# Optimization experiments

Hardware: AMD Instinct MI355X
Metric: run time of the kernel (lower is better)

Reference implementation:

```python
import jax, jax.numpy as jnp
import numpy as np

B, N, K = 8, 4096, 64          # graphs, nodes per graph, clusters
E_PER = 65536                   # edges per graph (avg degree 16)
EPS = 1e-15


def gcn_conv(x, W, b, src, dst, num_nodes):
    """PyG GCNConv: add self-loops, symmetric deg^-1/2 normalization, sum-aggregate at dst."""
    h = x @ W
    loop = jnp.arange(num_nodes, dtype=src.dtype)
    s_all = jnp.concatenate([src, loop])
    d_all = jnp.concatenate([dst, loop])
    deg = jax.ops.segment_sum(jnp.ones(d_all.shape[0], dtype=h.dtype), d_all, num_segments=num_nodes)
    dis = jnp.where(deg > 0, jax.lax.rsqrt(deg), 0.0)
    msg = h[s_all] * (dis[s_all] * dis[d_all])[:, None]
    return jax.ops.segment_sum(msg, d_all, num_segments=num_nodes) + b


def setup_inputs() -> dict:
    key = jax.random.key(0)
    ks = jax.random.split(key, 12)
    F_in, H, F_out = 128, 128, 128
    x = jax.random.normal(ks[0], (B * N, F_in), dtype=jnp.float32)
    # within-graph random edges, then offset to global node ids
    local = jax.random.randint(ks[1], (2, B * E_PER), 0, N, dtype=jnp.int32)
    offs = jnp.repeat(jnp.arange(B, dtype=jnp.int32) * N, E_PER)
    edge_index = local + offs[None, :]
    batch = jnp.repeat(jnp.arange(B, dtype=jnp.int32), N)

    def lin(k, i, o):
        return (jax.random.normal(k, (i, o), dtype=jnp.float32) / np.float32(np.sqrt(i)))

    return {
        "x": x, "edge_index": edge_index, "batch": batch,
        "W1": lin(ks[2], F_in, H), "b1": jnp.zeros((H,), jnp.float32),
        "W2": lin(ks[3], H, H),    "b2": jnp.zeros((H,), jnp.float32),
        "Wa1": lin(ks[4], H, H),   "ba1": jnp.zeros((H,), jnp.float32),
        "Wa2": lin(ks[5], H, K),   "ba2": jnp.zeros((K,), jnp.float32),
        "Wo": lin(ks[6], H, F_out), "bo": jnp.zeros((F_out,), jnp.float32),
    }


def reference(x, edge_index, batch, W1, b1, W2, b2, Wa1, ba1, Wa2, ba2, Wo, bo):
    num_nodes = B * N
    src, dst = edge_index[0], edge_index[1]
    # two GCN layers (dropout inactive in eval mode)
    h = jax.nn.relu(gcn_conv(x, W1, b1, src, dst, num_nodes))
    h = gcn_conv(h, W2, b2, src, dst, num_nodes)
    # assignment MLP + softmax (module applies softmax; dense_mincut_pool re-applies it)
    s = jax.nn.softmax(jnp.tanh(h @ Wa1 + ba1) @ Wa2 + ba2, axis=-1)
    # to_dense_adj: scatter edges into [B, N, N]
    g = src // N
    adj = jnp.zeros((B, N, N), h.dtype).at[g, src % N, dst % N].add(1.0)
    # to_dense_batch: equal-size graphs -> reshape (mask all True)
    x_d = h.reshape(B, N, -1)
    s_d = jax.nn.softmax(s.reshape(B, N, K), axis=-1)  # PyG internal softmax (double softmax, faithful)
    # dense_mincut_pool
    out = jnp.einsum('bnk,bnf->bkf', s_d, x_d)              # s^T x : [B,K,F]
    As = jnp.einsum('bnm,bmk->bnk', adj, s_d)
    out_adj = jnp.einsum('bnk,bnj->bkj', s_d, As)           # s^T A s : [B,K,K]
    mincut_num = jnp.trace(out_adj, axis1=-2, axis2=-1)
    d_flat = adj.sum(-1)                                    # node degrees
    mincut_den = jnp.einsum('bnk,bn,bnk->b', s_d, d_flat, s_d)  # trace(s^T D s)
    mincut_loss = jnp.mean(-(mincut_num / mincut_den))
    ss = jnp.einsum('bnk,bnj->bkj', s_d, s_d)
    ss_n = jnp.linalg.norm(ss, axis=(-1, -2), keepdims=True)
    i_s = jnp.eye(K, dtype=ss.dtype)
    ortho_loss = jnp.mean(jnp.linalg.norm(ss / ss_n - i_s / jnp.sqrt(jnp.float32(K)), axis=(-1, -2)))
    # zero diagonal + symmetric degree normalization of pooled adj
    out_adj = out_adj * (1.0 - i_s)
    d = jnp.sqrt(out_adj.sum(-1))[:, None, :] + EPS         # [B,1,K]
    out_adj = out_adj / d / jnp.swapaxes(d, 1, 2)
    # output projection
    pooled_x = jax.nn.relu(out.reshape(-1, out.shape[-1]) @ Wo + bo)  # [B*K, F_out]
    pooled_batch = jnp.repeat(jnp.arange(B), K)
    # pooled_adj returned densely: pooled_edge_index == nonzero(pooled_adj > 0) (dynamic shape)
    return pooled_x, out_adj, pooled_batch, mincut_loss, ortho_loss
```

## Files before the change

### kernel.cpp

```cpp
#include <hip/hip_runtime.h>

#define NNODES 32768
#define NEDGES 524288
#define KCL 64
#define CPG 16

typedef _Float16 half8v __attribute__((ext_vector_type(8)));
typedef _Float16 half4v __attribute__((ext_vector_type(4)));
typedef float floatx4 __attribute__((ext_vector_type(4)));

#define WT1_OFF   0
#define WT2_OFF   16384
#define WTA1_OFF  32768
#define WTA2_OFF  49152
#define WTO_OFF   57344
#define WT_TOTAL  73728

__device__ __forceinline__ float wave_sum(float v) {
#pragma unroll
  for (int off = 32; off > 0; off >>= 1) v += __shfl_xor(v, off, 64);
  return v;
}

__global__ __launch_bounds__(256) void histgemm1_kernel(const int* __restrict__ src, const int* __restrict__ dst,
                                                        int* __restrict__ pIn,
                                                        const float* __restrict__ W1, const float* __restrict__ W2,
                                                        const float* __restrict__ Wa1, const float* __restrict__ Wa2,
                                                        const float* __restrict__ Wo, _Float16* __restrict__ wt16,
                                                        const float* __restrict__ x, _Float16* __restrict__ h16A,
                                                        float* __restrict__ out) {
  __shared__ _Float16 WT[128][136];
  const int t = threadIdx.x;
  if (blockIdx.x < 128) {
    int* hIn = reinterpret_cast<int*>(&WT[0][0]);
    const int g = blockIdx.x & 7;
    const int chunk = blockIdx.x >> 3;
    const int ebase = (g << 16) + (chunk << 12);
    const int nbase = g << 12;
    if (blockIdx.x == 0 && t < 2) out[98816 + t] = 0.f;
    for (int i = t; i < 4096; i += 256) hIn[i] = 0;
    __syncthreads();
    {
      int tg = blockIdx.x * 256 + t;
#pragma unroll
      for (int i = 0; i < 3; i++) {
        int id = tg + i * 32768;
        if (id < WT_TOTAL) {
          const float* W; int base, BN;
          if (id < 16384)      { W = W1;  base = WT1_OFF;  BN = 128; }
          else if (id < 32768) { W = W2;  base = WT2_OFF;  BN = 128; }
          else if (id < 49152) { W = Wa1; base = WTA1_OFF; BN = 128; }
          else if (id < 57344) { W = Wa2; base = WTA2_OFF; BN = 64; }
          else                 { W = Wo;  base = WTO_OFF;  BN = 128; }
          int m = id - base;
          int k = m / BN, n = m % BN;
          wt16[base + n * 128 + k] = (_Float16)W[m];
        }
      }
    }
    const int4* dst4 = reinterpret_cast<const int4*>(dst + ebase);
#pragma unroll
    for (int i = 0; i < 4; ++i) {
      int4 d = dst4[i * 256 + t];
      atomicAdd(&hIn[d.x - nbase], 1);
      atomicAdd(&hIn[d.y - nbase], 1);
      atomicAdd(&hIn[d.z - nbase], 1);
      atomicAdd(&hIn[d.w - nbase], 1);
    }
    __syncthreads();
    int* dIn = pIn + ((size_t)(g * CPG + chunk) << 12);
    for (int i = t; i < 4096; i += 256) dIn[i] = hIn[i];
  } else {
    const int bid = blockIdx.x - 128;
    const int lane = t & 63;
    const int quad = lane >> 4, l16 = lane & 15;
    const long rowbase = (long)(bid & 7) * 4096 + (long)(bid >> 3) * 128 + (t >> 6) * 32;
    half8v af[2][4];
#pragma unroll
    for (int rt = 0; rt < 2; rt++)
#pragma unroll
      for (int kt = 0; kt < 4; kt++) {
        const float* p = x + (rowbase + rt * 16 + l16) * 128 + kt * 32 + quad * 8;
        float4 p0 = *reinterpret_cast<const float4*>(p);
        float4 p1 = *reinterpret_cast<const float4*>(p + 4);
        half8v h = {(_Float16)p0.x, (_Float16)p0.y, (_Float16)p0.z, (_Float16)p0.w,
                    (_Float16)p1.x, (_Float16)p1.y, (_Float16)p1.z, (_Float16)p1.w};
        af[rt][kt] = h;
      }
#pragma unroll
    for (int i = 0; i < 16; i++) {
      int idx = i * 256 + t;
      int k = idx >> 5, n4 = (idx & 31) << 2;
      float4 wv = *reinterpret_cast<const float4*>(W1 + k * 128 + n4);
      WT[n4 + 0][k] = (_Float16)wv.x;
      WT[n4 + 1][k] = (_Float16)wv.y;
      WT[n4 + 2][k] = (_Float16)wv.z;
      WT[n4 + 3][k] = (_Float16)wv.w;
    }
    __syncthreads();
    floatx4 acc[2][8];
#pragma unroll
    for (int rt = 0; rt < 2; rt++)
#pragma unroll
      for (int ct = 0; ct < 8; ct++) acc[rt][ct] = {0.f, 0.f, 0.f, 0.f};
#pragma unroll
    for (int kt = 0; kt < 4; kt++) {
      half8v bf[8];
#pragma unroll
      for (int ct = 0; ct < 8; ct++)
        bf[ct] = *reinterpret_cast<const half8v*>(&WT[ct * 16 + l16][kt * 32 + quad * 8]);
#pragma unroll
      for (int rt = 0; rt < 2; rt++)
#pragma unroll
        for (int ct = 0; ct < 8; ct++)
          acc[rt][ct] = __builtin_amdgcn_mfma_f32_16x16x32_f16(af[rt][kt], bf[ct], acc[rt][ct], 0, 0, 0);
    }
#pragma unroll
    for (int rt = 0; rt < 2; rt++) {
#pragma unroll
      for (int r = 0; r < 4; r++) {
        long row = rowbase + rt * 16 + quad * 4 + r;
#pragma unroll
        for (int ct = 0; ct < 8; ct++)
          h16A[row * 128 + ct * 16 + l16] = (_Float16)acc[rt][ct][r];
      }
    }
  }
}

__global__ __launch_bounds__(1024) void scan2_kernel(const int* __restrict__ pIn, int* __restrict__ offs,
                                                     int* __restrict__ cbase, float* __restrict__ dis) {
  __shared__ int part[1024];
  const int t = threadIdx.x;
  const int g = blockIdx.x;
  int tot[4];
  int s = 0;
#pragma unroll
  for (int j = 0; j < 4; ++j) {
    int l = t * 4 + j;
    int cnt = 0;
#pragma unroll
    for (int c = 0; c < CPG; ++c) cnt += pIn[(((size_t)(g * CPG + c)) << 12) + l];
    tot[j] = cnt;
    s += cnt;
  }
  part[t] = s;
  __syncthreads();
  for (int off = 1; off < 1024; off <<= 1) {
    int add = (t >= off) ? part[t - off] : 0;
    __syncthreads();
    part[t] += add;
    __syncthreads();
  }
  int run = (g << 16) + ((t == 0) ? 0 : part[t - 1]);
#pragma unroll
  for (int j = 0; j < 4; ++j) {
    int l = t * 4 + j;
    int n = (g << 12) + l;
    offs[n] = run;
    dis[n] = rsqrtf((float)tot[j] + 1.0f);
    int running = run;
#pragma unroll
    for (int c = 0; c < CPG; ++c) {
      size_t idx = (((size_t)(g * CPG + c)) << 12) + l;
      cbase[idx] = running;
      running += pIn[idx];
    }
    run += tot[j];
  }
  if (g == 0 && t == 0) offs[NNODES] = NEDGES;
}

__global__ __launch_bounds__(256) void scatter2_kernel(const int* __restrict__ src, const int* __restrict__ dst,
                                                       const int* __restrict__ cbase, int* __restrict__ ssrc) {
  __shared__ int cur[4096];
  const int t = threadIdx.x;
  const int g = blockIdx.x & 7;
  const int chunk = blockIdx.x >> 3;
  const int ebase = (g << 16) + (chunk << 12);
  const int nbase = g << 12;
  const int* cb = cbase + ((size_t)(g * CPG + chunk) << 12);
  for (int i = t; i < 4096; i += 256) cur[i] = cb[i];
  __syncthreads();
  const int4* dst4 = reinterpret_cast<const int4*>(dst + ebase);
  const int4* src4 = reinterpret_cast<const int4*>(src + ebase);
#pragma unroll
  for (int i = 0; i < 4; ++i) {
    int4 d = dst4[i * 256 + t];
    int4 s = src4[i * 256 + t];
    int p0 = atomicAdd(&cur[d.x - nbase], 1); ssrc[p0] = s.x;
    int p1 = atomicAdd(&cur[d.y - nbase], 1); ssrc[p1] = s.y;
    int p2 = atomicAdd(&cur[d.z - nbase], 1); ssrc[p2] = s.z;
    int p3 = atomicAdd(&cur[d.w - nbase], 1); ssrc[p3] = s.w;
  }
}

template <int ACT, int BIAS, int SCALE, int AFP32>
__global__ __launch_bounds__(256) void mgemm_kernel(const void* __restrict__ Ain, const _Float16* __restrict__ WT16,
                                                    const float* __restrict__ bias, const float* __restrict__ rowscale,
                                                    _Float16* __restrict__ Cout) {
  __shared__ _Float16 WT[128][136];
  const int t = threadIdx.x;
  const int lane = t & 63;
  const int quad = lane >> 4, l16 = lane & 15;
  const long rowbase = (long)(blockIdx.x & 7) * 4096 + (long)(blockIdx.x >> 3) * 128 + (t >> 6) * 32;
  half8v af[2][4];
#pragma unroll
  for (int rt = 0; rt < 2; rt++)
#pragma unroll
    for (int kt = 0; kt < 4; kt++) {
      if (AFP32) {
        const float* A32 = (const float*)Ain;
        const float* p = A32 + (rowbase + rt * 16 + l16) * 128 + kt * 32 + quad * 8;
        float4 p0 = *reinterpret_cast<const float4*>(p);
        float4 p1 = *reinterpret_cast<const float4*>(p + 4);
        half8v h = {(_Float16)p0.x, (_Float16)p0.y, (_Float16)p0.z, (_Float16)p0.w,
                    (_Float16)p1.x, (_Float16)p1.y, (_Float16)p1.z, (_Float16)p1.w};
        af[rt][kt] = h;
      } else {
        const _Float16* A16 = (const _Float16*)Ain;
        af[rt][kt] = *reinterpret_cast<const half8v*>(A16 + (rowbase + rt * 16 + l16) * 128 + kt * 32 + quad * 8);
      }
    }
#pragma unroll
  for (int i = 0; i < 8; i++) {
    int idx = i * 256 + t;
    int n = idx >> 4, k8 = (idx & 15) << 3;
    *reinterpret_cast<half8v*>(&WT[n][k8]) = *reinterpret_cast<const half8v*>(&WT16[n * 128 + k8]);
  }
  __syncthreads();
  floatx4 acc[2][8];
#pragma unroll
  for (int rt = 0; rt < 2; rt++)
#pragma unroll
    for (int ct = 0; ct < 8; ct++) acc[rt][ct] = {0.f, 0.f, 0.f, 0.f};
#pragma unroll
  for (int kt = 0; kt < 4; kt++) {
    half8v bf[8];
#pragma unroll
    for (int ct = 0; ct < 8; ct++)
      bf[ct] = *reinterpret_cast<const half8v*>(&WT[ct * 16 + l16][kt * 32 + quad * 8]);
#pragma unroll
    for (int rt = 0; rt < 2; rt++)
#pragma unroll
      for (int ct = 0; ct < 8; ct++)
        acc[rt][ct] = __builtin_amdgcn_mfma_f32_16x16x32_f16(af[rt][kt], bf[ct], acc[rt][ct], 0, 0, 0);
  }
#pragma unroll
  for (int rt = 0; rt < 2; rt++) {
#pragma unroll
    for (int r = 0; r < 4; r++) {
      long row = rowbase + rt * 16 + quad * 4 + r;
      float sc = SCALE ? rowscale[row] : 1.f;
#pragma unroll
      for (int ct = 0; ct < 8; ct++) {
        float v = acc[rt][ct][r];
        if (SCALE) v *= sc;
        if (BIAS) v += bias[ct * 16 + l16];
        if (ACT == 1) v = fmaxf(v, 0.f);
        Cout[row * 128 + ct * 16 + l16] = (_Float16)v;
      }
    }
  }
}

__global__ __launch_bounds__(256) void mlp_kernel(const _Float16* __restrict__ h2, const _Float16* __restrict__ wta1,
                                                  const _Float16* __restrict__ wta2, const float* __restrict__ ba1,
                                                  const float* __restrict__ ba2, _Float16* __restrict__ sh) {
  __shared__ _Float16 WT1[128][136];
  __shared__ _Float16 Z[64][136];
  const int t = threadIdx.x;
  const int lane = t & 63;
  const int quad = lane >> 4, l16 = lane & 15;
  const int w = t >> 6;
  const long rowbase = (long)(blockIdx.x & 7) * 4096 + (long)(blockIdx.x >> 3) * 64 + w * 16;
  half8v af[4];
#pragma unroll
  for (int kt = 0; kt < 4; kt++)
    af[kt] = *reinterpret_cast<const half8v*>(h2 + (rowbase + l16) * 128 + kt * 32 + quad * 8);
#pragma unroll
  for (int i = 0; i < 8; i++) {
    int idx = i * 256 + t;
    int n = idx >> 4, k8 = (idx & 15) << 3;
    *reinterpret_cast<half8v*>(&WT1[n][k8]) = *reinterpret_cast<const half8v*>(&wta1[n * 128 + k8]);
  }
  __syncthreads();
  {
    floatx4 acc[8];
#pragma unroll
    for (int ct = 0; ct < 8; ct++) acc[ct] = {0.f, 0.f, 0.f, 0.f};
#pragma unroll
    for (int kt = 0; kt < 4; kt++) {
#pragma unroll
      for (int ct = 0; ct < 8; ct++) {
        half8v bf = *reinterpret_cast<const half8v*>(&WT1[ct * 16 + l16][kt * 32 + quad * 8]);
        acc[ct] = __builtin_amdgcn_mfma_f32_16x16x32_f16(af[kt], bf, acc[ct], 0, 0, 0);
      }
    }
#pragma unroll
    for (int r = 0; r < 4; r++) {
      int lrow = w * 16 + quad * 4 + r;
#pragma unroll
      for (int ct = 0; ct < 8; ct++) {
        float zx = acc[ct][r] + ba1[ct * 16 + l16];
        float ex = __expf(2.0f * zx);
        float v = 1.0f - 2.0f * __builtin_amdgcn_rcpf(ex + 1.0f);
        Z[lrow][ct * 16 + l16] = (_Float16)v;
      }
    }
  }
  __syncthreads();
#pragma unroll
  for (int i = 0; i < 4; i++) {
    int idx = i * 256 + t;
    int n = idx >> 4, k8 = (idx & 15) << 3;
    *reinterpret_cast<half8v*>(&WT1[n][k8]) = *reinterpret_cast<const half8v*>(&wta2[n * 128 + k8]);
  }
  half8v af2[4];
#pragma unroll
  for (int kt = 0; kt < 4; kt++)
    af2[kt] = *reinterpret_cast<const half8v*>(&Z[w * 16 + l16][kt * 32 + quad * 8]);
  __syncthreads();
  floatx4 acc2[4];
#pragma unroll
  for (int ct = 0; ct < 4; ct++) acc2[ct] = {0.f, 0.f, 0.f, 0.f};
#pragma unroll
  for (int kt = 0; kt < 4; kt++) {
#pragma unroll
    for (int ct = 0; ct < 4; ct++) {
      half8v bf = *reinterpret_cast<const half8v*>(&WT1[ct * 16 + l16][kt * 32 + quad * 8]);
      acc2[ct] = __builtin_amdgcn_mfma_f32_16x16x32_f16(af2[kt], bf, acc2[ct], 0, 0, 0);
    }
  }
#pragma unroll
  for (int r = 0; r < 4; r++) {
    long row = rowbase + quad * 4 + r;
    float v[4];
#pragma unroll
    for (int ct = 0; ct < 4; ct++) v[ct] = acc2[ct][r] + ba2[ct * 16 + l16];
    float m = fmaxf(fmaxf(v[0], v[1]), fmaxf(v[2], v[3]));
#pragma unroll
    for (int off = 1; off <= 8; off <<= 1) m = fmaxf(m, __shfl_xor(m, off, 64));
    float se = 0.f;
#pragma unroll
    for (int ct = 0; ct < 4; ct++) { v[ct] = __expf(v[ct] - m); se += v[ct]; }
#pragma unroll
    for (int off = 1; off <= 8; off <<= 1) se += __shfl_xor(se, off, 64);
    float inv = 1.0f / se;
#pragma unroll
    for (int ct = 0; ct < 4; ct++) v[ct] *= inv;
    float m2 = fmaxf(fmaxf(v[0], v[1]), fmaxf(v[2], v[3]));
#pragma unroll
    for (int off = 1; off <= 8; off <<= 1) m2 = fmaxf(m2, __shfl_xor(m2, off, 64));
    float se2 = 0.f;
#pragma unroll
    for (int ct = 0; ct < 4; ct++) { v[ct] = __expf(v[ct] - m2); se2 += v[ct]; }
#pragma unroll
    for (int off = 1; off <= 8; off <<= 1) se2 += __shfl_xor(se2, off, 64);
    float inv2 = 1.0f / se2;
#pragma unroll
    for (int ct = 0; ct < 4; ct++) sh[row * 64 + ct * 16 + l16] = (_Float16)(v[ct] * inv2);
  }
}

template <int RELU, int DISSRC>
__global__ __launch_bounds__(256) void aggregate_kernel(const _Float16* __restrict__ hs, const float* __restrict__ dis,
                                                        const int* __restrict__ offs, const int* __restrict__ ssrc,
                                                        const float* __restrict__ bias, _Float16* __restrict__ outh) {
  const int lane = threadIdx.x & 63;
  const int b = blockIdx.x;
  const int node = ((b & 7) << 12) + ((b >> 3) << 2) + (threadIdx.x >> 6);
  const int q = lane >> 4;
  const int fl = (lane & 15) * 8;
  const int e0 = offs[node], e1 = offs[node + 1];
  const float dn = dis[node];
  float fa[8];
#pragma unroll
  for (int j = 0; j < 8; j++) fa[j] = 0.f;
  int e = e0;
  for (; e + 16 <= e1; e += 16) {
    int s0 = ssrc[e + q];
    int s1 = ssrc[e + 4 + q];
    int s2 = ssrc[e + 8 + q];
    int s3 = ssrc[e + 12 + q];
    float d0 = 1.f, d1 = 1.f, d2 = 1.f, d3 = 1.f;
    if (DISSRC) { d0 = dis[s0]; d1 = dis[s1]; d2 = dis[s2]; d3 = dis[s3]; }
    half8v v0 = *reinterpret_cast<const half8v*>(hs + (size_t)s0 * 128 + fl);
    half8v v1 = *reinterpret_cast<const half8v*>(hs + (size_t)s1 * 128 + fl);
    half8v v2 = *reinterpret_cast<const half8v*>(hs + (size_t)s2 * 128 + fl);
    half8v v3 = *reinterpret_cast<const half8v*>(hs + (size_t)s3 * 128 + fl);
#pragma unroll
    for (int j = 0; j < 8; j++) {
      if (DISSRC) {
        fa[j] = fmaf(d0, (float)v0[j], fa[j]);
        fa[j] = fmaf(d1, (float)v1[j], fa[j]);
        fa[j] = fmaf(d2, (float)v2[j], fa[j]);
        fa[j] = fmaf(d3, (float)v3[j], fa[j]);
      } else {
        fa[j] += (float)v0[j] + (float)v1[j] + (float)v2[j] + (float)v3[j];
      }
    }
  }
  if (e < e1) {
    int last = e1 - 1;
    int s[4]; bool m[4];
#pragma unroll
    for (int jj = 0; jj < 4; jj++) {
      int idx = e + jj * 4 + q;
      m[jj] = idx < e1;
      int sv = ssrc[idx < last ? idx : last];
      s[jj] = m[jj] ? sv : node;
    }
#pragma unroll
    for (int jj = 0; jj < 4; jj++) {
      half8v v = *reinterpret_cast<const half8v*>(hs + (size_t)s[jj] * 128 + fl);
      float ds = DISSRC ? dis[s[jj]] : 1.f;
      if (m[jj]) {
#pragma unroll
        for (int j = 0; j < 8; j++) {
          if (DISSRC) fa[j] = fmaf(ds, (float)v[j], fa[j]);
          else fa[j] += (float)v[j];
        }
      }
    }
  }
#pragma unroll
  for (int j = 0; j < 8; j++) {
    fa[j] += __shfl_xor(fa[j], 16, 64);
    fa[j] += __shfl_xor(fa[j], 32, 64);
  }
  if (q == 0) {
    half8v self = *reinterpret_cast<const half8v*>(hs + (size_t)node * 128 + fl);
    float4 b0 = *reinterpret_cast<const float4*>(bias + fl);
    float4 b1 = *reinterpret_cast<const float4*>(bias + fl + 4);
    float bb[8] = {b0.x, b0.y, b0.z, b0.w, b1.x, b1.y, b1.z, b1.w};
    half8v r;
#pragma unroll
    for (int j = 0; j < 8; j++) {
      float acc = fa[j];
      if (DISSRC) acc = fmaf(dn, (float)self[j], acc);
      else acc += (float)self[j];
      float v = fmaf(acc, dn, bb[j]);
      if (RELU) v = fmaxf(v, 0.f);
      r[j] = (_Float16)v;
    }
    *reinterpret_cast<half8v*>(outh + (size_t)node * 128 + fl) = r;
  }
}

__global__ __launch_bounds__(256) void gather_kernel(const _Float16* __restrict__ sh, const int* __restrict__ offs,
                                                     const int* __restrict__ ssrc, _Float16* __restrict__ Gh,
                                                     float* __restrict__ dnp) {
  const int lane = threadIdx.x & 63;
  const int b = blockIdx.x;
  const int node = ((b & 7) << 12) + ((b >> 3) << 2) + (threadIdx.x >> 6);
  const int q = lane >> 3;
  const int fl = (lane & 7) * 8;
  const int e0 = offs[node], e1 = offs[node + 1];
  float fa[8];
  float sq = 0.f;
#pragma unroll
  for (int j = 0; j < 8; j++) fa[j] = 0.f;
  int e = e0;
  for (; e + 16 <= e1; e += 16) {
    int s0 = ssrc[e + q];
    int s1 = ssrc[e + 8 + q];
    half8v v0 = *reinterpret_cast<const half8v*>(sh + (size_t)s0 * 64 + fl);
    half8v v1 = *reinterpret_cast<const half8v*>(sh + (size_t)s1 * 64 + fl);
#pragma unroll
    for (int j = 0; j < 8; j++) {
      float f0 = (float)v0[j], f1 = (float)v1[j];
      fa[j] += f0 + f1;
      sq = fmaf(f0, f0, sq);
      sq = fmaf(f1, f1, sq);
    }
  }
  if (e < e1) {
    int last = e1 - 1;
    int i0 = e + q, i1 = e + 8 + q;
    bool m0 = i0 < e1, m1 = i1 < e1;
    int sv0 = ssrc[i0 < last ? i0 : last];
    int sv1 = ssrc[i1 < last ? i1 : last];
    int s0 = m0 ? sv0 : node;
    int s1 = m1 ? sv1 : node;
    half8v v0 = *reinterpret_cast<const half8v*>(sh + (size_t)s0 * 64 + fl);
    half8v v1 = *reinterpret_cast<const half8v*>(sh + (size_t)s1 * 64 + fl);
#pragma unroll
    for (int j = 0; j < 8; j++) {
      float f0 = m0 ? (float)v0[j] : 0.f;
      float f1 = m1 ? (float)v1[j] : 0.f;
      fa[j] += f0 + f1;
      sq = fmaf(f0, f0, sq);
      sq = fmaf(f1, f1, sq);
    }
  }
#pragma unroll
  for (int j = 0; j < 8; j++) {
    fa[j] += __shfl_xor(fa[j], 8, 64);
    fa[j] += __shfl_xor(fa[j], 16, 64);
    fa[j] += __shfl_xor(fa[j], 32, 64);
  }
  float den = wave_sum(sq);
  if (lane == 0) dnp[node] = den;
  if (q == 0) {
    half8v r;
#pragma unroll
    for (int j = 0; j < 8; j++) r[j] = (_Float16)fa[j];
    *reinterpret_cast<half8v*>(Gh + (size_t)node * 64 + fl) = r;
  }
}

__global__ __launch_bounds__(512) void atb_kernel(const _Float16* __restrict__ sh, const _Float16* __restrict__ Gh,
                                                  const _Float16* __restrict__ h2, float* __restrict__ pF) {
  __shared__ _Float16 XsT[64][136];
  __shared__ _Float16 YsT[256][40];
  const int t = threadIdx.x;
  const int g = blockIdx.x & 7, chunk = blockIdx.x >> 3;
  const int n0 = g * 4096 + chunk * 128;
  const int lane = t & 63;
  const int w = t >> 6;
  const int mtile = w & 3;
  const int nhalf = w >> 2;
  const int quad = lane >> 4, l16 = lane & 15;

#pragma unroll
  for (int i = 0; i < 4; i++) {
    int slot = i * 512 + t;
    int k = slot >> 4, c4 = (slot & 15) * 4;
    half4v v = *reinterpret_cast<const half4v*>(&sh[(size_t)(n0 + k) * 64 + c4]);
#pragma unroll
    for (int j = 0; j < 4; j++) XsT[c4 + j][k] = v[j];
  }

  floatx4 acc[8];
#pragma unroll
  for (int nt = 0; nt < 8; nt++) acc[nt] = {0.f, 0.f, 0.f, 0.f};

  for (int kt = 0; kt < 4; ++kt) {
    const int nb = n0 + kt * 32;
    __syncthreads();
#pragma unroll
    for (int i = 0; i < 4; i++) {
      int slot = i * 512 + t;
      int cg = slot & 15, k = (slot >> 4) & 31, ch = slot >> 9;
      int c = ch * 64 + cg * 4;
      half4v v;
      if (c < 64)       v = *reinterpret_cast<const half4v*>(&Gh[(size_t)(nb + k) * 64 + c]);
      else if (c < 128) v = *reinterpret_cast<const half4v*>(&sh[(size_t)(nb + k) * 64 + (c - 64)]);
      else              v = *reinterpret_cast<const half4v*>(&h2[(size_t)(nb + k) * 128 + (c - 128)]);
#pragma unroll
      for (int j = 0; j < 4; j++) YsT[c + j][k] = v[j];
    }
    __syncthreads();
    half8v af = *reinterpret_cast<const half8v*>(&XsT[mtile * 16 + l16][kt * 32 + quad * 8]);
#pragma unroll
    for (int nt = 0; nt < 8; nt++) {
      half8v bf = *reinterpret_cast<const half8v*>(&YsT[(nhalf * 8 + nt) * 16 + l16][quad * 8]);
      acc[nt] = __builtin_amdgcn_mfma_f32_16x16x32_f16(af, bf, acc[nt], 0, 0, 0);
    }
  }
  float* dst = pF + (size_t)blockIdx.x * 16384;
#pragma unroll
  for (int nt = 0; nt < 8; nt++) {
#pragma unroll
    for (int r = 0; r < 4; r++) {
      dst[(mtile * 16 + quad * 4 + r) * 256 + (nhalf * 8 + nt) * 16 + l16] = acc[nt][r];
    }
  }
}

__global__ __launch_bounds__(256) void merge_kernel(const float* __restrict__ pF, float* __restrict__ oadj,
                                                    float* __restrict__ ssb, _Float16* __restrict__ outp16) {
  int g = blockIdx.x & 7;
  int o4 = (blockIdx.x >> 3) * 256 + threadIdx.x;
  float sx = 0.f, sy = 0.f, sz = 0.f, sw = 0.f;
#pragma unroll
  for (int q = 0; q < 32; ++q) {
    float4 v = *reinterpret_cast<const float4*>(pF + (size_t)(q * 8 + g) * 16384 + o4 * 4);
    sx += v.x; sy += v.y; sz += v.z; sw += v.w;
  }
  int row = o4 >> 6;
  int c = (o4 & 63) * 4;
  if (c < 64) {
    float4 o = {sx, sy, sz, sw};
    *reinterpret_cast<float4*>(&oadj[g * 4096 + row * 64 + c]) = o;
  } else if (c < 128) {
    float4 o = {sx, sy, sz, sw};
    *reinterpret_cast<float4*>(&ssb[g * 4096 + row * 64 + (c - 64)]) = o;
  } else {
    half4v h = {(_Float16)sx, (_Float16)sy, (_Float16)sz, (_Float16)sw};
    *reinterpret_cast<half4v*>(&outp16[g * 8192 + row * 128 + (c - 128)]) = h;
  }
}

__global__ __launch_bounds__(256) void epilogue2_kernel(const float* __restrict__ oadj, const float* __restrict__ ssb,
                                                        const _Float16* __restrict__ outp16, const _Float16* __restrict__ wto,
                                                        const float* __restrict__ bo, const float* __restrict__ dn,
                                                        float* __restrict__ out) {
  __shared__ _Float16 outpS[64][136];
  __shared__ _Float16 WoT[128][136];
  __shared__ float red[256];
  __shared__ float rowsum[64];
  __shared__ float dw[4], w1[4], w2[4], w3[4];
  const int g = blockIdx.x, t = threadIdx.x;

#pragma unroll
  for (int i = 0; i < 8; i++) {
    int idx = i * 256 + t;
    int n = idx >> 4, k8 = (idx & 15) << 3;
    *reinterpret_cast<half8v*>(&WoT[n][k8]) = *reinterpret_cast<const half8v*>(&wto[n * 128 + k8]);
  }
#pragma unroll
  for (int i = 0; i < 4; i++) {
    int idx = i * 256 + t;
    int orow = idx >> 4, c8 = (idx & 15) * 8;
    half8v v = *reinterpret_cast<const half8v*>(&outp16[g * 8192 + orow * 128 + c8]);
    *reinterpret_cast<half8v*>(&outpS[orow][c8]) = v;
  }

  const int row = t >> 2, p = t & 3;
  float Areg[16];
  float trs_p = 0.f, ssq_p = 0.f;
#pragma unroll
  for (int c4 = 0; c4 < 4; c4++) {
    float4 a = *reinterpret_cast<const float4*>(&oadj[g * 4096 + row * 64 + p * 16 + c4 * 4]);
    Areg[c4 * 4 + 0] = a.x; Areg[c4 * 4 + 1] = a.y; Areg[c4 * 4 + 2] = a.z; Areg[c4 * 4 + 3] = a.w;
    float4 s = *reinterpret_cast<const float4*>(&ssb[g * 4096 + row * 64 + p * 16 + c4 * 4]);
    float vv[4] = {s.x, s.y, s.z, s.w};
#pragma unroll
    for (int jj = 0; jj < 4; jj++) {
      ssq_p += vv[jj] * vv[jj];
      int col = p * 16 + c4 * 4 + jj;
      if (col == row) trs_p += vv[jj];
    }
  }
  float da = 0.f;
#pragma unroll
  for (int i = 0; i < 16; i++) da += dn[g * 4096 + i * 256 + t];
  float dws = wave_sum(da);
  if ((t & 63) == 0) dw[t >> 6] = dws;

  float rs = 0.f, tra = 0.f;
#pragma unroll
  for (int c = 0; c < 16; c++) {
    int j = p * 16 + c;
    if (j == row) tra += Areg[c];
    else rs += Areg[c];
  }
  red[t] = rs;
  __syncthreads();
  if (p == 0) rowsum[row] = red[t] + red[t + 1] + red[t + 2] + red[t + 3];
  float v1 = wave_sum(tra), v2 = wave_sum(trs_p), v3 = wave_sum(ssq_p);
  if ((t & 63) == 0) { int w = t >> 6; w1[w] = v1; w2[w] = v2; w3[w] = v3; }
  __syncthreads();
  if (t == 0) {
    float TRA = w1[0] + w1[1] + w1[2] + w1[3];
    float TRS = w2[0] + w2[1] + w2[2] + w2[3];
    float SSQ = w3[0] + w3[1] + w3[2] + w3[3];
    float DEN = dw[0] + dw[1] + dw[2] + dw[3];
    atomicAdd(&out[98816], -(TRA / DEN) * 0.125f);
    float ssn = sqrtf(SSQ);
    atomicAdd(&out[98817], sqrtf(2.0f - TRS / (4.0f * ssn)) * 0.125f);
  }
  float di = sqrtf(rowsum[row]) + 1e-15f;
#pragma unroll
  for (int c = 0; c < 16; c++) {
    int j = p * 16 + c;
    float v = (j == row) ? 0.f : Areg[c];
    float dj = sqrtf(rowsum[j]) + 1e-15f;
    out[65536 + g * 4096 + row * 64 + j] = v / (di * dj);
  }
  if (t < 64) out[98304 + g * 64 + t] = (float)g;

  const int lane = t & 63;
  const int quad = lane >> 4, l16 = lane & 15;
  const int w = t >> 6;
  floatx4 acc[8];
#pragma unroll
  for (int ct = 0; ct < 8; ct++) acc[ct] = {0.f, 0.f, 0.f, 0.f};
#pragma unroll
  for (int kt = 0; kt < 4; kt++) {
    half8v af = *reinterpret_cast<const half8v*>(&outpS[w * 16 + l16][kt * 32 + quad * 8]);
#pragma unroll
    for (int ct = 0; ct < 8; ct++) {
      half8v bf = *reinterpret_cast<const half8v*>(&WoT[ct * 16 + l16][kt * 32 + quad * 8]);
      acc[ct] = __builtin_amdgcn_mfma_f32_16x16x32_f16(af, bf, acc[ct], 0, 0, 0);
    }
  }
#pragma unroll
  for (int r = 0; r < 4; r++) {
    int orow = w * 16 + quad * 4 + r;
#pragma unroll
    for (int ct = 0; ct < 8; ct++) {
      int col = ct * 16 + l16;
      float v = fmaxf(acc[ct][r] + bo[col], 0.f);
      out[(g * 64 + orow) * 128 + col] = v;
    }
  }
}

extern "C" void kernel_launch(void* const* d_in, const int* in_sizes, int n_in,
                              void* d_out, int out_size, void* d_ws, size_t ws_size,
                              hipStream_t stream) {
  const float* x   = (const float*)d_in[0];
  const int*   ei  = (const int*)d_in[1];
  const float* W1  = (const float*)d_in[3];
  const float* b1  = (const float*)d_in[4];
  const float* W2  = (const float*)d_in[5];
  const float* b2  = (const float*)d_in[6];
  const float* Wa1 = (const float*)d_in[7];
  const float* ba1 = (const float*)d_in[8];
  const float* Wa2 = (const float*)d_in[9];
  const float* ba2 = (const float*)d_in[10];
  const float* Wo  = (const float*)d_in[11];
  const float* bo  = (const float*)d_in[12];
  const int* src = ei;
  const int* dst = ei + NEDGES;
  float* out = (float*)d_out;

  char* ws = (char*)d_ws;
  size_t o = 0;
  auto alloc = [&](size_t bytes) -> void* {
    void* p = ws + o;
    o += (bytes + 255) & ~(size_t)255;
    return p;
  };
  _Float16* h16A = (_Float16*)alloc((size_t)NNODES * 128 * 2);
  _Float16* h16B = (_Float16*)alloc((size_t)NNODES * 128 * 2);
  _Float16* h16C = (_Float16*)alloc((size_t)NNODES * 128 * 2);
  _Float16* sh   = (_Float16*)alloc((size_t)NNODES * 64 * 2);
  _Float16* Gh   = (_Float16*)alloc((size_t)NNODES * 64 * 2);
  float* pF    = (float*)alloc((size_t)256 * 16384 * 4);
  float* dis   = (float*)alloc((size_t)NNODES * 4);
  int* offs    = (int*)alloc((size_t)(NNODES + 1) * 4);
  int* ssrc    = (int*)alloc((size_t)NEDGES * 4);
  int* pIn     = (int*)alloc((size_t)8 * CPG * 4096 * 4);
  int* cbase   = (int*)alloc((size_t)8 * CPG * 4096 * 4);
  float* dn    = (float*)alloc((size_t)NNODES * 4);
  float* oadj  = (float*)alloc(8 * 4096 * 4);
  float* ssb   = (float*)alloc(8 * 4096 * 4);
  _Float16* outp16 = (_Float16*)alloc(8 * 8192 * 2);
  _Float16* wt16   = (_Float16*)alloc((size_t)WT_TOTAL * 2);

  histgemm1_kernel<<<384, 256, 0, stream>>>(src, dst, pIn, W1, W2, Wa1, Wa2, Wo, wt16, x, h16A, out);
  scan2_kernel<<<8, 1024, 0, stream>>>(pIn, offs, cbase, dis);
  scatter2_kernel<<<8 * CPG, 256, 0, stream>>>(src, dst, cbase, ssrc);

  aggregate_kernel<1, 1><<<NNODES / 4, 256, 0, stream>>>(h16A, dis, offs, ssrc, b1, h16B);
  mgemm_kernel<0, 0, 1, 0><<<NNODES / 128, 256, 0, stream>>>(h16B, wt16 + WT2_OFF, nullptr, dis, h16A);
  aggregate_kernel<0, 0><<<NNODES / 4, 256, 0, stream>>>(h16A, dis, offs, ssrc, b2, h16C);

  mlp_kernel<<<NNODES / 64, 256, 0, stream>>>(h16C, wt16 + WTA1_OFF, wt16 + WTA2_OFF, ba1, ba2, sh);

  gather_kernel<<<NNODES / 4, 256, 0, stream>>>(sh, offs, ssrc, Gh, dn);
  atb_kernel<<<256, 512, 0, stream>>>(sh, Gh, h16C, pF);
  merge_kernel<<<128, 256, 0, stream>>>(pF, oadj, ssb, outp16);
  epilogue2_kernel<<<8, 256, 0, stream>>>(oadj, ssb, outp16, wt16 + WTO_OFF, bo, dn, out);
}
```

Baseline: 194.0 us.

## Fuse sparse aggregations with following GEMMs, MLP, and pooling A^T B

Fuses layer-1 aggregation with the W2 GEMM, layer-2 aggregation with the assignment MLP, and the neighbor gather of s with the pooling A^T B kernel. Intermediates (aggregated features, gathered Gh) now stay in shared memory instead of round-tripping through global memory, and three kernel launches are removed. In exchange, each block processes many nodes serially, with one wave per node per iteration, so parallelism drops to 512 or 256 blocks. Latency-bound gathers may be hidden less well than in the previous 8192-block kernels.

```diff
diff --git a/kernel.cpp b/kernel.cpp
--- a/kernel.cpp
+++ b/kernel.cpp
@@ -195,121 +195,226 @@
   }
 }
 
-template <int ACT, int BIAS, int SCALE, int AFP32>
-__global__ __launch_bounds__(256) void mgemm_kernel(const void* __restrict__ Ain, const _Float16* __restrict__ WT16,
-                                                    const float* __restrict__ bias, const float* __restrict__ rowscale,
-                                                    _Float16* __restrict__ Cout) {
+__global__ __launch_bounds__(512) void agg1gemm2_kernel(const _Float16* __restrict__ hs, const float* __restrict__ dis,
+                                                        const int* __restrict__ offs, const int* __restrict__ ssrc,
+                                                        const float* __restrict__ bias, const _Float16* __restrict__ wt2,
+                                                        _Float16* __restrict__ outh) {
+  __shared__ _Float16 H[64][136];
   __shared__ _Float16 WT[128][136];
   const int t = threadIdx.x;
   const int lane = t & 63;
+  const int w = t >> 6;
   const int quad = lane >> 4, l16 = lane & 15;
-  const long rowbase = (long)(blockIdx.x & 7) * 4096 + (long)(blockIdx.x >> 3) * 128 + (t >> 6) * 32;
-  half8v af[2][4];
-#pragma unroll
-  for (int rt = 0; rt < 2; rt++)
-#pragma unroll
-    for (int kt = 0; kt < 4; kt++) {
-      if (AFP32) {
-        const float* A32 = (const float*)Ain;
-        const float* p = A32 + (rowbase + rt * 16 + l16) * 128 + kt * 32 + quad * 8;
-        float4 p0 = *reinterpret_cast<const float4*>(p);
-        float4 p1 = *reinterpret_cast<const float4*>(p + 4);
-        half8v h = {(_Float16)p0.x, (_Float16)p0.y, (_Float16)p0.z, (_Float16)p0.w,
-                    (_Float16)p1.x, (_Float16)p1.y, (_Float16)p1.z, (_Float16)p1.w};
-        af[rt][kt] = h;
-      } else {
-        const _Float16* A16 = (const _Float16*)Ain;
-        af[rt][kt] = *reinterpret_cast<const half8v*>(A16 + (rowbase + rt * 16 + l16) * 128 + kt * 32 + quad * 8);
-      }
-    }
-#pragma unroll
-  for (int i = 0; i < 8; i++) {
-    int idx = i * 256 + t;
+  const int fl = l16 * 8;
+  const long rowbase0 = (long)(blockIdx.x & 7) * 4096 + (long)(blockIdx.x >> 3) * 64;
+#pragma unroll
+  for (int i = 0; i < 4; i++) {
+    int idx = i * 512 + t;
     int n = idx >> 4, k8 = (idx & 15) << 3;
-    *reinterpret_cast<half8v*>(&WT[n][k8]) = *reinterpret_cast<const half8v*>(&WT16[n * 128 + k8]);
+    *reinterpret_cast<half8v*>(&WT[n][k8]) = *reinterpret_cast<const half8v*>(&wt2[n * 128 + k8]);
+  }
+  for (int nn = 0; nn < 8; nn++) {
+    const int local = w + nn * 8;
+    const int node = (int)(rowbase0 + local);
+    const int e0 = offs[node], e1 = offs[node + 1];
+    const float dn = dis[node];
+    float fa[8];
+#pragma unroll
+    for (int j = 0; j < 8; j++) fa[j] = 0.f;
+    int e = e0;
+    for (; e + 16 <= e1; e += 16) {
+      int s0 = ssrc[e + quad];
+      int s1 = ssrc[e + 4 + quad];
+      int s2 = ssrc[e + 8 + quad];
+      int s3 = ssrc[e + 12 + quad];
+      float d0 = dis[s0], d1 = dis[s1], d2 = dis[s2], d3 = dis[s3];
+      half8v v0 = *reinterpret_cast<const half8v*>(hs + (size_t)s0 * 128 + fl);
+      half8v v1 = *reinterpret_cast<const half8v*>(hs + (size_t)s1 * 128 + fl);
+      half8v v2 = *reinterpret_cast<const half8v*>(hs + (size_t)s2 * 128 + fl);
+      half8v v3 = *reinterpret_cast<const half8v*>(hs + (size_t)s3 * 128 + fl);
+#pragma unroll
+      for (int j = 0; j < 8; j++) {
+        fa[j] = fmaf(d0, (float)v0[j], fa[j]);
+        fa[j] = fmaf(d1, (float)v1[j], fa[j]);
+        fa[j] = fmaf(d2, (float)v2[j], fa[j]);
+        fa[j] = fmaf(d3, (float)v3[j], fa[j]);
+      }
+    }
+    if (e < e1) {
+      int last = e1 - 1;
+      int s[4]; bool m[4];
+#pragma unroll
+      for (int jj = 0; jj < 4; jj++) {
+        int idx = e + jj * 4 + quad;
+        m[jj] = idx < e1;
+        int sv = ssrc[idx < last ? idx : last];
+        s[jj] = m[jj] ? sv : node;
+      }
+#pragma unroll
+      for (int jj = 0; jj < 4; jj++) {
+        half8v v = *reinterpret_cast<const half8v*>(hs + (size_t)s[jj] * 128 + fl);
+        float ds = dis[s[jj]];
+        if (m[jj]) {
+#pragma unroll
+          for (int j = 0; j < 8; j++) fa[j] = fmaf(ds, (float)v[j], fa[j]);
+        }
+      }
+    }
+#pragma unroll
+    for (int j = 0; j < 8; j++) {
+      fa[j] += __shfl_xor(fa[j], 16, 64);
+      fa[j] += __shfl_xor(fa[j], 32, 64);
+    }
+    if (quad == 0) {
+      half8v self = *reinterpret_cast<const half8v*>(hs + (size_t)node * 128 + fl);
+      float4 b0 = *reinterpret_cast<const float4*>(bias + fl);
+      float4 b1v = *reinterpret_cast<const float4*>(bias + fl + 4);
+      float bb[8] = {b0.x, b0.y, b0.z, b0.w, b1v.x, b1v.y, b1v.z, b1v.w};
+#pragma unroll
+      for (int j = 0; j < 8; j++) {
+        float acc = fmaf(dn, (float)self[j], fa[j]);
+        float v = fmaf(acc, dn, bb[j]);
+        v = fmaxf(v, 0.f);
+        H[local][fl + j] = (_Float16)v;
+      }
+    }
   }
   __syncthreads();
-  floatx4 acc[2][8];
-#pragma unroll
-  for (int rt = 0; rt < 2; rt++)
-#pragma unroll
-    for (int ct = 0; ct < 8; ct++) acc[rt][ct] = {0.f, 0.f, 0.f, 0.f};
+  const int mtile = w & 3, nhalf = w >> 2;
+  half8v af[4];
+#pragma unroll
+  for (int kt = 0; kt < 4; kt++)
+    af[kt] = *reinterpret_cast<const half8v*>(&H[mtile * 16 + l16][kt * 32 + quad * 8]);
+  floatx4 acc[4];
+#pragma unroll
+  for (int ct = 0; ct < 4; ct++) acc[ct] = {0.f, 0.f, 0.f, 0.f};
 #pragma unroll
   for (int kt = 0; kt < 4; kt++) {
-    half8v bf[8];
-#pragma unroll
-    for (int ct = 0; ct < 8; ct++)
-      bf[ct] = *reinterpret_cast<const half8v*>(&WT[ct * 16 + l16][kt * 32 + quad * 8]);
-#pragma unroll
-    for (int rt = 0; rt < 2; rt++)
-#pragma unroll
-      for (int ct = 0; ct < 8; ct++)
-        acc[rt][ct] = __builtin_amdgcn_mfma_f32_16x16x32_f16(af[rt][kt], bf[ct], acc[rt][ct], 0, 0, 0);
-  }
-#pragma unroll
-  for (int rt = 0; rt < 2; rt++) {
-#pragma unroll
-    for (int r = 0; r < 4; r++) {
-      long row = rowbase + rt * 16 + quad * 4 + r;
-      float sc = SCALE ? rowscale[row] : 1.f;
-#pragma unroll
-      for (int ct = 0; ct < 8; ct++) {
-        float v = acc[rt][ct][r];
-        if (SCALE) v *= sc;
-        if (BIAS) v += bias[ct * 16 + l16];
-        if (ACT == 1) v = fmaxf(v, 0.f);
-        Cout[row * 128 + ct * 16 + l16] = (_Float16)v;
-      }
-    }
-  }
-}
-
-__global__ __launch_bounds__(256) void mlp_kernel(const _Float16* __restrict__ h2, const _Float16* __restrict__ wta1,
-                                                  const _Float16* __restrict__ wta2, const float* __restrict__ ba1,
-                                                  const float* __restrict__ ba2, _Float16* __restrict__ sh) {
+#pragma unroll
+    for (int ct = 0; ct < 4; ct++) {
+      half8v bf = *reinterpret_cast<const half8v*>(&WT[(nhalf * 4 + ct) * 16 + l16][kt * 32 + quad * 8]);
+      acc[ct] = __builtin_amdgcn_mfma_f32_16x16x32_f16(af[kt], bf, acc[ct], 0, 0, 0);
+    }
+  }
+#pragma unroll
+  for (int r = 0; r < 4; r++) {
+    long row = rowbase0 + mtile * 16 + quad * 4 + r;
+    float sc = dis[row];
+#pragma unroll
+    for (int ct = 0; ct < 4; ct++)
+      outh[row * 128 + (nhalf * 4 + ct) * 16 + l16] = (_Float16)(acc[ct][r] * sc);
+  }
+}
+
+__global__ __launch_bounds__(256) void agg2mlp_kernel(const _Float16* __restrict__ hs, const float* __restrict__ dis,
+                                                      const int* __restrict__ offs, const int* __restrict__ ssrc,
+                                                      const float* __restrict__ b2, const _Float16* __restrict__ wta1,
+                                                      const _Float16* __restrict__ wta2, const float* __restrict__ ba1,
+                                                      const float* __restrict__ ba2, _Float16* __restrict__ h16C,
+                                                      _Float16* __restrict__ sh) {
   __shared__ _Float16 WT1[128][136];
-  __shared__ _Float16 Z[64][136];
+  __shared__ _Float16 HZ[64][136];
   const int t = threadIdx.x;
   const int lane = t & 63;
   const int quad = lane >> 4, l16 = lane & 15;
   const int w = t >> 6;
-  const long rowbase = (long)(blockIdx.x & 7) * 4096 + (long)(blockIdx.x >> 3) * 64 + w * 16;
-  half8v af[4];
-#pragma unroll
-  for (int kt = 0; kt < 4; kt++)
-    af[kt] = *reinterpret_cast<const half8v*>(h2 + (rowbase + l16) * 128 + kt * 32 + quad * 8);
+  const int fl = l16 * 8;
+  const long rowbase0 = (long)(blockIdx.x & 7) * 4096 + (long)(blockIdx.x >> 3) * 64;
 #pragma unroll
   for (int i = 0; i < 8; i++) {
     int idx = i * 256 + t;
     int n = idx >> 4, k8 = (idx & 15) << 3;
     *reinterpret_cast<half8v*>(&WT1[n][k8]) = *reinterpret_cast<const half8v*>(&wta1[n * 128 + k8]);
   }
+  for (int nn = 0; nn < 16; nn++) {
+    const int local = w + nn * 4;
+    const int node = (int)(rowbase0 + local);
+    const int e0 = offs[node], e1 = offs[node + 1];
+    const float dn = dis[node];
+    float fa[8];
+#pragma unroll
+    for (int j = 0; j < 8; j++) fa[j] = 0.f;
+    int e = e0;
+    for (; e + 16 <= e1; e += 16) {
+      int s0 = ssrc[e + quad];
+      int s1 = ssrc[e + 4 + quad];
+      int s2 = ssrc[e + 8 + quad];
+      int s3 = ssrc[e + 12 + quad];
+      half8v v0 = *reinterpret_cast<const half8v*>(hs + (size_t)s0 * 128 + fl);
+      half8v v1 = *reinterpret_cast<const half8v*>(hs + (size_t)s1 * 128 + fl);
+      half8v v2 = *reinterpret_cast<const half8v*>(hs + (size_t)s2 * 128 + fl);
+      half8v v3 = *reinterpret_cast<const half8v*>(hs + (size_t)s3 * 128 + fl);
+#pragma unroll
+      for (int j = 0; j < 8; j++) fa[j] += (float)v0[j] + (float)v1[j] + (float)v2[j] + (float)v3[j];
+    }
+    if (e < e1) {
+      int last = e1 - 1;
+      int s[4]; bool m[4];
+#pragma unroll
+      for (int jj = 0; jj < 4; jj++) {
+        int idx = e + jj * 4 + quad;
+        m[jj] = idx < e1;
+        int sv = ssrc[idx < last ? idx : last];
+        s[jj] = m[jj] ? sv : node;
+      }
+#pragma unroll
+      for (int jj = 0; jj < 4; jj++) {
+        half8v v = *reinterpret_cast<const half8v*>(hs + (size_t)s[jj] * 128 + fl);
+        if (m[jj]) {
+#pragma unroll
+          for (int j = 0; j < 8; j++) fa[j] += (float)v[j];
+        }
+      }
+    }
+#pragma unroll
+    for (int j = 0; j < 8; j++) {
+      fa[j] += __shfl_xor(fa[j], 16, 64);
+      fa[j] += __shfl_xor(fa[j], 32, 64);
+    }
+    if (quad == 0) {
+      half8v self = *reinterpret_cast<const half8v*>(hs + (size_t)node * 128 + fl);
+      float4 b0 = *reinterpret_cast<const float4*>(b2 + fl);
+      float4 b1v = *reinterpret_cast<const float4*>(b2 + fl + 4);
+      float bb[8] = {b0.x, b0.y, b0.z, b0.w, b1v.x, b1v.y, b1v.z, b1v.w};
+      half8v r;
+#pragma unroll
+      for (int j = 0; j < 8; j++) {
+        float acc = fa[j] + (float)self[j];
+        float v = fmaf(acc, dn, bb[j]);
+        r[j] = (_Float16)v;
+      }
+      *reinterpret_cast<half8v*>(&HZ[local][fl]) = r;
+      *reinterpret_cast<half8v*>(h16C + (size_t)node * 128 + fl) = r;
+    }
+  }
   __syncthreads();
-  {
-    floatx4 acc[8];
-#pragma unroll
-    for (int ct = 0; ct < 8; ct++) acc[ct] = {0.f, 0.f, 0.f, 0.f};
-#pragma unroll
-    for (int kt = 0; kt < 4; kt++) {
-#pragma unroll
-      for (int ct = 0; ct < 8; ct++) {
-        half8v bf = *reinterpret_cast<const half8v*>(&WT1[ct * 16 + l16][kt * 32 + quad * 8]);
-        acc[ct] = __builtin_amdgcn_mfma_f32_16x16x32_f16(af[kt], bf, acc[ct], 0, 0, 0);
-      }
-    }
-#pragma unroll
-    for (int r = 0; r < 4; r++) {
-      int lrow = w * 16 + quad * 4 + r;
-#pragma unroll
-      for (int ct = 0; ct < 8; ct++) {
-        float zx = acc[ct][r] + ba1[ct * 16 + l16];
-        float ex = __expf(2.0f * zx);
-        float v = 1.0f - 2.0f * __builtin_amdgcn_rcpf(ex + 1.0f);
-        Z[lrow][ct * 16 + l16] = (_Float16)v;
-      }
+  half8v af[4];
+#pragma unroll
+  for (int kt = 0; kt < 4; kt++)
+    af[kt] = *reinterpret_cast<const half8v*>(&HZ[w * 16 + l16][kt * 32 + quad * 8]);
+  floatx4 acc[8];
+#pragma unroll
+  for (int ct = 0; ct < 8; ct++) acc[ct] = {0.f, 0.f, 0.f, 0.f};
+#pragma unroll
+  for (int kt = 0; kt < 4; kt++) {
+#pragma unroll
+    for (int ct = 0; ct < 8; ct++) {
+      half8v bf = *reinterpret_cast<const half8v*>(&WT1[ct * 16 + l16][kt * 32 + quad * 8]);
+      acc[ct] = __builtin_amdgcn_mfma_f32_16x16x32_f16(af[kt], bf, acc[ct], 0, 0, 0);
     }
   }
   __syncthreads();
+#pragma unroll
+  for (int r = 0; r < 4; r++) {
+    int lrow = w * 16 + quad * 4 + r;
+#pragma unroll
+    for (int ct = 0; ct < 8; ct++) {
+      float zx = acc[ct][r] + ba1[ct * 16 + l16];
+      float ex = __expf(2.0f * zx);
+      float v = 1.0f - 2.0f * __builtin_amdgcn_rcpf(ex + 1.0f);
+      HZ[lrow][ct * 16 + l16] = (_Float16)v;
+    }
+  }
 #pragma unroll
   for (int i = 0; i < 4; i++) {
     int idx = i * 256 + t;
@@ -319,7 +424,7 @@
   half8v af2[4];
 #pragma unroll
   for (int kt = 0; kt < 4; kt++)
-    af2[kt] = *reinterpret_cast<const half8v*>(&Z[w * 16 + l16][kt * 32 + quad * 8]);
+    af2[kt] = *reinterpret_cast<const half8v*>(&HZ[w * 16 + l16][kt * 32 + quad * 8]);
   __syncthreads();
   floatx4 acc2[4];
 #pragma unroll
@@ -334,7 +439,7 @@
   }
 #pragma unroll
   for (int r = 0; r < 4; r++) {
-    long row = rowbase + quad * 4 + r;
+    long row = rowbase0 + w * 16 + quad * 4 + r;
     float v[4];
 #pragma unroll
     for (int ct = 0; ct < 4; ct++) v[ct] = acc2[ct][r] + ba2[ct * 16 + l16];
@@ -363,166 +468,75 @@
   }
 }
 
-template <int RELU, int DISSRC>
-__global__ __launch_bounds__(256) void aggregate_kernel(const _Float16* __restrict__ hs, const float* __restrict__ dis,
+__global__ __launch_bounds__(512) void gatheratb_kernel(const _Float16* __restrict__ sh, const _Float16* __restrict__ h2,
                                                         const int* __restrict__ offs, const int* __restrict__ ssrc,
-                                                        const float* __restrict__ bias, _Float16* __restrict__ outh) {
-  const int lane = threadIdx.x & 63;
-  const int b = blockIdx.x;
-  const int node = ((b & 7) << 12) + ((b >> 3) << 2) + (threadIdx.x >> 6);
-  const int q = lane >> 4;
-  const int fl = (lane & 15) * 8;
-  const int e0 = offs[node], e1 = offs[node + 1];
-  const float dn = dis[node];
-  float fa[8];
-#pragma unroll
-  for (int j = 0; j < 8; j++) fa[j] = 0.f;
-  int e = e0;
-  for (; e + 16 <= e1; e += 16) {
-    int s0 = ssrc[e + q];
-    int s1 = ssrc[e + 4 + q];
-    int s2 = ssrc[e + 8 + q];
-    int s3 = ssrc[e + 12 + q];
-    float d0 = 1.f, d1 = 1.f, d2 = 1.f, d3 = 1.f;
-    if (DISSRC) { d0 = dis[s0]; d1 = dis[s1]; d2 = dis[s2]; d3 = dis[s3]; }
-    half8v v0 = *reinterpret_cast<const half8v*>(hs + (size_t)s0 * 128 + fl);
-    half8v v1 = *reinterpret_cast<const half8v*>(hs + (size_t)s1 * 128 + fl);
-    half8v v2 = *reinterpret_cast<const half8v*>(hs + (size_t)s2 * 128 + fl);
-    half8v v3 = *reinterpret_cast<const half8v*>(hs + (size_t)s3 * 128 + fl);
-#pragma unroll
-    for (int j = 0; j < 8; j++) {
-      if (DISSRC) {
-        fa[j] = fmaf(d0, (float)v0[j], fa[j]);
-        fa[j] = fmaf(d1, (float)v1[j], fa[j]);
-        fa[j] = fmaf(d2, (float)v2[j], fa[j]);
-        fa[j] = fmaf(d3, (float)v3[j], fa[j]);
-      } else {
-        fa[j] += (float)v0[j] + (float)v1[j] + (float)v2[j] + (float)v3[j];
-      }
-    }
-  }
-  if (e < e1) {
-    int last = e1 - 1;
-    int s[4]; bool m[4];
-#pragma unroll
-    for (int jj = 0; jj < 4; jj++) {
-      int idx = e + jj * 4 + q;
-      m[jj] = idx < e1;
-      int sv = ssrc[idx < last ? idx : last];
-      s[jj] = m[jj] ? sv : node;
-    }
-#pragma unroll
-    for (int jj = 0; jj < 4; jj++) {
-      half8v v = *reinterpret_cast<const half8v*>(hs + (size_t)s[jj] * 128 + fl);
-      float ds = DISSRC ? dis[s[jj]] : 1.f;
-      if (m[jj]) {
-#pragma unroll
-        for (int j = 0; j < 8; j++) {
-          if (DISSRC) fa[j] = fmaf(ds, (float)v[j], fa[j]);
-          else fa[j] += (float)v[j];
-        }
-      }
-    }
-  }
-#pragma unroll
-  for (int j = 0; j < 8; j++) {
-    fa[j] += __shfl_xor(fa[j], 16, 64);
-    fa[j] += __shfl_xor(fa[j], 32, 64);
-  }
-  if (q == 0) {
-    half8v self = *reinterpret_cast<const half8v*>(hs + (size_t)node * 128 + fl);
-    float4 b0 = *reinterpret_cast<const float4*>(bias + fl);
-    float4 b1 = *reinterpret_cast<const float4*>(bias + fl + 4);
-    float bb[8] = {b0.x, b0.y, b0.z, b0.w, b1.x, b1.y, b1.z, b1.w};
-    half8v r;
-#pragma unroll
-    for (int j = 0; j < 8; j++) {
-      float acc = fa[j];
-      if (DISSRC) acc = fmaf(dn, (float)self[j], acc);
-      else acc += (float)self[j];
-      float v = fmaf(acc, dn, bb[j]);
-      if (RELU) v = fmaxf(v, 0.f);
-      r[j] = (_Float16)v;
-    }
-    *reinterpret_cast<half8v*>(outh + (size_t)node * 128 + fl) = r;
-  }
-}
-
-__global__ __launch_bounds__(256) void gather_kernel(const _Float16* __restrict__ sh, const int* __restrict__ offs,
-                                                     const int* __restrict__ ssrc, _Float16* __restrict__ Gh,
-                                                     float* __restrict__ dnp) {
-  const int lane = threadIdx.x & 63;
-  const int b = blockIdx.x;
-  const int node = ((b & 7) << 12) + ((b >> 3) << 2) + (threadIdx.x >> 6);
-  const int q = lane >> 3;
-  const int fl = (lane & 7) * 8;
-  const int e0 = offs[node], e1 = offs[node + 1];
-  float fa[8];
-  float sq = 0.f;
-#pragma unroll
-  for (int j = 0; j < 8; j++) fa[j] = 0.f;
-  int e = e0;
-  for (; e + 16 <= e1; e += 16) {
-    int s0 = ssrc[e + q];
-    int s1 = ssrc[e + 8 + q];
-    half8v v0 = *reinterpret_cast<const half8v*>(sh + (size_t)s0 * 64 + fl);
-    half8v v1 = *reinterpret_cast<const half8v*>(sh + (size_t)s1 * 64 + fl);
-#pragma unroll
-    for (int j = 0; j < 8; j++) {
-      float f0 = (float)v0[j], f1 = (float)v1[j];
-      fa[j] += f0 + f1;
-      sq = fmaf(f0, f0, sq);
-      sq = fmaf(f1, f1, sq);
-    }
-  }
-  if (e < e1) {
-    int last = e1 - 1;
-    int i0 = e + q, i1 = e + 8 + q;
-    bool m0 = i0 < e1, m1 = i1 < e1;
-    int sv0 = ssrc[i0 < last ? i0 : last];
-    int sv1 = ssrc[i1 < last ? i1 : last];
-    int s0 = m0 ? sv0 : node;
-    int s1 = m1 ? sv1 : node;
-    half8v v0 = *reinterpret_cast<const half8v*>(sh + (size_t)s0 * 64 + fl);
-    half8v v1 = *reinterpret_cast<const half8v*>(sh + (size_t)s1 * 64 + fl);
-#pragma unroll
-    for (int j = 0; j < 8; j++) {
-      float f0 = m0 ? (float)v0[j] : 0.f;
-      float f1 = m1 ? (float)v1[j] : 0.f;
-      fa[j] += f0 + f1;
-      sq = fmaf(f0, f0, sq);
-      sq = fmaf(f1, f1, sq);
-    }
-  }
-#pragma unroll
-  for (int j = 0; j < 8; j++) {
-    fa[j] += __shfl_xor(fa[j], 8, 64);
-    fa[j] += __shfl_xor(fa[j], 16, 64);
-    fa[j] += __shfl_xor(fa[j], 32, 64);
-  }
-  float den = wave_sum(sq);
-  if (lane == 0) dnp[node] = den;
-  if (q == 0) {
-    half8v r;
-#pragma unroll
-    for (int j = 0; j < 8; j++) r[j] = (_Float16)fa[j];
-    *reinterpret_cast<half8v*>(Gh + (size_t)node * 64 + fl) = r;
-  }
-}
-
-__global__ __launch_bounds__(512) void atb_kernel(const _Float16* __restrict__ sh, const _Float16* __restrict__ Gh,
-                                                  const _Float16* __restrict__ h2, float* __restrict__ pF) {
+                                                        float* __restrict__ dnp, float* __restrict__ pF) {
+  __shared__ _Float16 YG[128][80];
   __shared__ _Float16 XsT[64][136];
   __shared__ _Float16 YsT[256][40];
   const int t = threadIdx.x;
+  const int lane = t & 63;
+  const int w = t >> 6;
   const int g = blockIdx.x & 7, chunk = blockIdx.x >> 3;
   const int n0 = g * 4096 + chunk * 128;
-  const int lane = t & 63;
-  const int w = t >> 6;
-  const int mtile = w & 3;
-  const int nhalf = w >> 2;
-  const int quad = lane >> 4, l16 = lane & 15;
-
+  const int q8 = lane >> 3;
+  const int fl8 = (lane & 7) * 8;
+  for (int nn = 0; nn < 16; nn++) {
+    const int local = w + nn * 8;
+    const int node = n0 + local;
+    const int e0 = offs[node], e1 = offs[node + 1];
+    float fa[8];
+    float sq = 0.f;
+#pragma unroll
+    for (int j = 0; j < 8; j++) fa[j] = 0.f;
+    int e = e0;
+    for (; e + 16 <= e1; e += 16) {
+      int s0 = ssrc[e + q8];
+      int s1 = ssrc[e + 8 + q8];
+      half8v v0 = *reinterpret_cast<const half8v*>(sh + (size_t)s0 * 64 + fl8);
+      half8v v1 = *reinterpret_cast<const half8v*>(sh + (size_t)s1 * 64 + fl8);
+#pragma unroll
+      for (int j = 0; j < 8; j++) {
+        float f0 = (float)v0[j], f1 = (float)v1[j];
+        fa[j] += f0 + f1;
+        sq = fmaf(f0, f0, sq);
+        sq = fmaf(f1, f1, sq);
+      }
+    }
+    if (e < e1) {
+      int last = e1 - 1;
+      int i0 = e + q8, i1 = e + 8 + q8;
+      bool m0 = i0 < e1, m1 = i1 < e1;
+      int sv0 = ssrc[i0 < last ? i0 : last];
+      int sv1 = ssrc[i1 < last ? i1 : last];
+      int s0 = m0 ? sv0 : node;
+      int s1 = m1 ? sv1 : node;
+      half8v v0 = *reinterpret_cast<const half8v*>(sh + (size_t)s0 * 64 + fl8);
+      half8v v1 = *reinterpret_cast<const half8v*>(sh + (size_t)s1 * 64 + fl8);
+#pragma unroll
+      for (int j = 0; j < 8; j++) {
+        float f0 = m0 ? (float)v0[j] : 0.f;
+        float f1 = m1 ? (float)v1[j] : 0.f;
+        fa[j] += f0 + f1;
+        sq = fmaf(f0, f0, sq);
+        sq = fmaf(f1, f1, sq);
+      }
+    }
+#pragma unroll
+    for (int j = 0; j < 8; j++) {
+      fa[j] += __shfl_xor(fa[j], 8, 64);
+      fa[j] += __shfl_xor(fa[j], 16, 64);
+      fa[j] += __shfl_xor(fa[j], 32, 64);
+    }
+    float den = wave_sum(sq);
+    if (lane == 0) dnp[node] = den;
+    if (q8 == 0) {
+      half8v r;
+#pragma unroll
+      for (int j = 0; j < 8; j++) r[j] = (_Float16)fa[j];
+      *reinterpret_cast<half8v*>(&YG[local][fl8]) = r;
+    }
+  }
 #pragma unroll
   for (int i = 0; i < 4; i++) {
     int slot = i * 512 + t;
@@ -531,11 +545,12 @@
 #pragma unroll
     for (int j = 0; j < 4; j++) XsT[c4 + j][k] = v[j];
   }
-
+  const int mtile = w & 3;
+  const int nhalf = w >> 2;
+  const int quad = lane >> 4, l16 = lane & 15;
   floatx4 acc[8];
 #pragma unroll
   for (int nt = 0; nt < 8; nt++) acc[nt] = {0.f, 0.f, 0.f, 0.f};
-
   for (int kt = 0; kt < 4; ++kt) {
     const int nb = n0 + kt * 32;
     __syncthreads();
@@ -545,7 +560,7 @@
       int cg = slot & 15, k = (slot >> 4) & 31, ch = slot >> 9;
       int c = ch * 64 + cg * 4;
       half4v v;
-      if (c < 64)       v = *reinterpret_cast<const half4v*>(&Gh[(size_t)(nb + k) * 64 + c]);
+      if (c < 64)       v = *reinterpret_cast<const half4v*>(&YG[kt * 32 + k][c]);
       else if (c < 128) v = *reinterpret_cast<const half4v*>(&sh[(size_t)(nb + k) * 64 + (c - 64)]);
       else              v = *reinterpret_cast<const half4v*>(&h2[(size_t)(nb + k) * 128 + (c - 128)]);
 #pragma unroll
@@ -729,7 +744,6 @@
   _Float16* h16B = (_Float16*)alloc((size_t)NNODES * 128 * 2);
   _Float16* h16C = (_Float16*)alloc((size_t)NNODES * 128 * 2);
   _Float16* sh   = (_Float16*)alloc((size_t)NNODES * 64 * 2);
-  _Float16* Gh   = (_Float16*)alloc((size_t)NNODES * 64 * 2);
   float* pF    = (float*)alloc((size_t)256 * 16384 * 4);
   float* dis   = (float*)alloc((size_t)NNODES * 4);
   int* offs    = (int*)alloc((size_t)(NNODES + 1) * 4);
@@ -745,15 +759,9 @@
   histgemm1_kernel<<<384, 256, 0, stream>>>(src, dst, pIn, W1, W2, Wa1, Wa2, Wo, wt16, x, h16A, out);
   scan2_kernel<<<8, 1024, 0, stream>>>(pIn, offs, cbase, dis);
   scatter2_kernel<<<8 * CPG, 256, 0, stream>>>(src, dst, cbase, ssrc);
-
-  aggregate_kernel<1, 1><<<NNODES / 4, 256, 0, stream>>>(h16A, dis, offs, ssrc, b1, h16B);
-  mgemm_kernel<0, 0, 1, 0><<<NNODES / 128, 256, 0, stream>>>(h16B, wt16 + WT2_OFF, nullptr, dis, h16A);
-  aggregate_kernel<0, 0><<<NNODES / 4, 256, 0, stream>>>(h16A, dis, offs, ssrc, b2, h16C);
-
-  mlp_kernel<<<NNODES / 64, 256, 0, stream>>>(h16C, wt16 + WTA1_OFF, wt16 + WTA2_OFF, ba1, ba2, sh);
-
-  gather_kernel<<<NNODES / 4, 256, 0, stream>>>(sh, offs, ssrc, Gh, dn);
-  atb_kernel<<<256, 512, 0, stream>>>(sh, Gh, h16C, pF);
+  agg1gemm2_kernel<<<512, 512, 0, stream>>>(h16A, dis, offs, ssrc, b1, wt16 + WT2_OFF, h16B);
+  agg2mlp_kernel<<<512, 256, 0, stream>>>(h16B, dis, offs, ssrc, b2, wt16 + WTA1_OFF, wt16 + WTA2_OFF, ba1, ba2, h16C, sh);
+  gatheratb_kernel<<<256, 512, 0, stream>>>(sh, h16C, offs, ssrc, dn, pF);
   merge_kernel<<<128, 256, 0, stream>>>(pF, oadj, ssb, outp16);
   epilogue2_kernel<<<8, 256, 0, stream>>>(oadj, ssb, outp16, wt16 + WTO_OFF, bo, dn, out);
 }
```

Result: slower. 206.7 us (+6.6%).
